# Kernel optimization log

Hardware: AMD Instinct MI355X
Metric: run time of the kernel (lower is better)

Reference implementation:

```python
import jax, jax.numpy as jnp
import numpy as np

BITS = 4
OFF = 8          # 2**(BITS-1)
QLEVELS = 15.0   # 2**BITS - 1
IN_F, OUT_F, FP_F, TOKENS = 4096, 4096, 256, 4096
INT_F = IN_F - FP_F


def unpack_i4(w_packed):
    """Invert pack_to_i4: packed uint8 col k holds signed int4 cols (2k: low nibble, 2k+1: high)."""
    lo = (w_packed & 0x0F).astype(jnp.int8)
    hi = ((w_packed >> 4) & 0x0F).astype(jnp.int8)
    lo = jnp.where(lo >= 8, lo - 16, lo)
    hi = jnp.where(hi >= 8, hi - 16, hi)
    return jnp.stack([lo, hi], axis=-1).reshape(w_packed.shape[0], -1)  # (out, int_features)


def setup_inputs() -> dict:
    key = jax.random.key(0)
    k1, k2, k3, k4, k5 = jax.random.split(key, 5)
    x = jax.random.normal(k1, (1, TOKENS, IN_F), dtype=jnp.float16)
    perm = jax.random.permutation(k2, IN_F)
    fp_indices = jnp.sort(perm[:FP_F]).astype(jnp.int64)
    int_indices = jnp.sort(perm[FP_F:]).astype(jnp.int64)
    # signed int4 weight values in [-8, 7], packed two-per-byte like pack_to_i4
    w_vals = jax.random.randint(k3, (OUT_F, INT_F), -8, 8, dtype=jnp.int8)
    u = (w_vals.astype(jnp.int32) & 0x0F).astype(jnp.uint8)
    int_weight = (u[:, 0::2] | (u[:, 1::2] << 4)).astype(jnp.uint8)  # (out, INT_F//2)
    weights_scales = (jax.random.uniform(k4, (OUT_F, 1)) * 0.01 + 1e-3).astype(jnp.float16)
    # reduced_w = row-sum of the dequantized int-column weights (as in from_float)
    reduced_w = (w_vals.astype(jnp.float32).sum(axis=1, keepdims=True)
                 * weights_scales.astype(jnp.float32)).T.astype(jnp.float16)  # (1, out)
    fp_weight = (jax.random.normal(k5, (OUT_F, FP_F)) * 0.02).astype(jnp.float16)
    bias = jnp.zeros((OUT_F,), dtype=jnp.float16)
    return {"x": x, "int_weight": int_weight, "weights_scales": weights_scales,
            "reduced_w": reduced_w, "fp_weight": fp_weight, "bias": bias,
            "int_indices": int_indices, "fp_indices": fp_indices}


def reference(x, int_weight, weights_scales, reduced_w, fp_weight, bias,
              int_indices, fp_indices):
    x2 = x[0]                                   # (M, in_features)
    int_x = x2[:, int_indices].astype(jnp.float32)   # (M, INT_F)
    fp_x = x2[:, fp_indices].astype(jnp.float32)     # (M, FP_F)
    # asymmetric per-row quantization to signed int4
    mn = int_x.min(axis=1, keepdims=True)
    mx = int_x.max(axis=1, keepdims=True)
    scale = jnp.maximum((mx - mn) / QLEVELS, 1e-8)   # (M,1)
    zero = mn                                        # (M,1)
    q = jnp.clip(jnp.round((int_x - zero) / scale) - OFF, -8, 7).astype(jnp.int8)
    w_int = unpack_i4(int_weight)                    # (out, INT_F) int8
    int_result = jnp.matmul(q.astype(jnp.int32), w_int.T.astype(jnp.int32))  # (M, out) int32
    fp_result = fp_x @ fp_weight.T.astype(jnp.float32) + bias.astype(jnp.float32)
    # asym dequant: x ~ (q + OFF)*scale + zero, W = w_int * w_scale, sum_j W_j = reduced_w
    w_scale = weights_scales.astype(jnp.float32)[:, 0][None, :]   # (1, out)
    out = (scale * w_scale * int_result.astype(jnp.float32)
           + (zero + scale * OFF) * reduced_w.astype(jnp.float32)
           + fp_result)
    return out.astype(jnp.float16)[None]             # (1, M, out)
```

## Files before the change

### kernel.cpp

```cpp
#include <hip/hip_runtime.h>
#include <hip/hip_bf16.h>

#define IN_FEAT 4096
#define OUT_FEAT 4096
#define FP_FEAT 256
#define INT_FEAT 3840
#define TOKENS 4096
#define PACKED_W (INT_FEAT / 2)

#define NT_I8 60
#define NT_ALL 68

typedef __attribute__((ext_vector_type(8))) short short8;
typedef __attribute__((ext_vector_type(4))) float f32x4;
typedef __attribute__((ext_vector_type(4))) int   int32x4;

#define AQ8_OFF   0u
#define WB8_OFF   16777216u
#define AFP_OFF   33554432u
#define WFP_OFF   35651584u
#define SCALE_OFF 37748736u
#define ZERO_OFF  37765120u
#define WS_NEED   37781504u

__global__ __launch_bounds__(256) void prep_kernel(
    const float* __restrict__ x,
    const int* __restrict__ int_idx_raw,
    const int* __restrict__ fp_idx_raw,
    const int* __restrict__ wpacked_raw,
    const float* __restrict__ fpw,
    const float* __restrict__ wscale,
    signed char* __restrict__ Aq8,
    __hip_bfloat16* __restrict__ Afp,
    signed char* __restrict__ Wb8,
    __hip_bfloat16* __restrict__ Wfp,
    float* __restrict__ scale_ws,
    float* __restrict__ zero_ws)
{
    const int t = threadIdx.x;
    if (blockIdx.x < TOKENS) {
        const int m = blockIdx.x;
        const float* xr = x + (size_t)m * IN_FEAT;
        const bool is64 = (int_idx_raw[1] == 0) && (int_idx_raw[3] == 0);

        float v[15];
        float mn = 1e30f, mx = -1e30f;
#pragma unroll
        for (int j = 0; j < 15; ++j) {
            int k = t + j * 256;
            int idx = is64 ? int_idx_raw[2 * k] : int_idx_raw[k];
            float f = xr[idx];
            v[j] = f;
            mn = fminf(mn, f);
            mx = fmaxf(mx, f);
        }
#pragma unroll
        for (int off = 1; off < 64; off <<= 1) {
            mn = fminf(mn, __shfl_xor(mn, off));
            mx = fmaxf(mx, __shfl_xor(mx, off));
        }
        __shared__ float smn[4], smx[4];
        int wid = t >> 6, lane = t & 63;
        if (lane == 0) { smn[wid] = mn; smx[wid] = mx; }
        __syncthreads();
        if (t == 0) {
            float rmn = fminf(fminf(smn[0], smn[1]), fminf(smn[2], smn[3]));
            float rmx = fmaxf(fmaxf(smx[0], smx[1]), fmaxf(smx[2], smx[3]));
            float sc = fmaxf((rmx - rmn) / 15.0f, 1e-8f);
            smn[0] = rmn;
            smx[0] = sc;
            scale_ws[m] = sc;
            zero_ws[m] = rmn;
        }
        __syncthreads();
        const float zero = smn[0];
        const float sc = smx[0];

        signed char* ar = Aq8 + (size_t)m * INT_FEAT;
#pragma unroll
        for (int j = 0; j < 15; ++j) {
            int k = t + j * 256;
            float q = rintf((v[j] - zero) / sc) - 8.0f;
            q = fminf(fmaxf(q, -8.0f), 7.0f);
            ar[k] = (signed char)(int)q;
        }
        int fpi = is64 ? fp_idx_raw[2 * t] : fp_idx_raw[t];
        Afp[(size_t)m * FP_FEAT + t] = __float2bfloat16(xr[fpi] / sc);
    } else {
        const int n = blockIdx.x - TOKENS;
        bool is_i32 = true;
#pragma unroll
        for (int j = 0; j < 8; ++j) {
            unsigned w = (unsigned)wpacked_raw[j];
            if (w > 0xFFu) is_i32 = false;
        }
        short* wo = (short*)(Wb8 + (size_t)n * INT_FEAT);
#pragma unroll
        for (int j = 0; j < 8; ++j) {
            int k = t + j * 256;
            if (k < PACKED_W) {
                int p = is_i32 ? wpacked_raw[(size_t)n * PACKED_W + k]
                               : ((const unsigned char*)wpacked_raw)[(size_t)n * PACKED_W + k];
                int lo = p & 15; if (lo >= 8) lo -= 16;
                int hi = (p >> 4) & 15; if (hi >= 8) hi -= 16;
                wo[k] = (short)(((unsigned char)lo) | ((unsigned short)(unsigned char)hi << 8));
            }
        }
        float wsn = wscale[n];
        Wfp[(size_t)n * FP_FEAT + t] = __float2bfloat16(fpw[(size_t)n * FP_FEAT + t] / wsn);
    }
}


__global__ __launch_bounds__(512, 2) void gemm256_i8(
    const signed char* __restrict__ Aq8,
    const __hip_bfloat16* __restrict__ Afp,
    const signed char* __restrict__ Wb8,
    const __hip_bfloat16* __restrict__ Wfp,
    const float* __restrict__ scale_ws,
    const float* __restrict__ zero_ws,
    const float* __restrict__ wscale,
    const float* __restrict__ reduced,
    const float* __restrict__ bias,
    float* __restrict__ out)
{
    __shared__ __align__(16) char lds[131072];

    const int t = threadIdx.x;
    const int lane = t & 63, wid = t >> 6;
    const int wr = wid >> 2;
    const int wc = wid & 3;
    const int r16 = lane & 15;
    const int kg = lane >> 4;

    const int bid = blockIdx.x;
    const int sb = (bid & 7) * 32 + (bid >> 3);
    const int tileM = (sb >> 4) * 256;
    const int tileN = (sb & 15) * 256;

    const int id0 = t, id1 = 512 + t;
    const int r0 = id0 >> 2, c0 = id0 & 3;
    const int r1 = id1 >> 2, c1 = id1 & 3;
    const int sw0 = ((c0 ^ ((r0 >> 1) & 3)) << 4);
    const int sw1 = ((c1 ^ ((r1 >> 1) & 3)) << 4);
    const char* a8_0 = (const char*)Aq8 + (size_t)(tileM + r0) * INT_FEAT + sw0;
    const char* a8_1 = (const char*)Aq8 + (size_t)(tileM + r1) * INT_FEAT + sw1;
    const char* b8_0 = (const char*)Wb8 + (size_t)(tileN + r0) * INT_FEAT + sw0;
    const char* b8_1 = (const char*)Wb8 + (size_t)(tileN + r1) * INT_FEAT + sw1;
    const char* af_0 = (const char*)Afp + (size_t)(tileM + r0) * 512 + sw0;
    const char* af_1 = (const char*)Afp + (size_t)(tileM + r1) * 512 + sw1;
    const char* bf_0 = (const char*)Wfp + (size_t)(tileN + r0) * 512 + sw0;
    const char* bf_1 = (const char*)Wfp + (size_t)(tileN + r1) * 512 + sw1;
    const int dst0 = id0 << 4, dst1 = id1 << 4;

    auto stage = [&](int vt, int bufB) {
        const char *pa0, *pa1, *pb0, *pb1;
        if (vt < NT_I8) {
            int ko = vt * 64;
            pa0 = a8_0 + ko; pa1 = a8_1 + ko; pb0 = b8_0 + ko; pb1 = b8_1 + ko;
        } else {
            int ko = (vt - NT_I8) * 64;
            pa0 = af_0 + ko; pa1 = af_1 + ko; pb0 = bf_0 + ko; pb1 = bf_1 + ko;
        }
        __builtin_amdgcn_global_load_lds(
            (const __attribute__((address_space(1))) void*)pa0,
            (__attribute__((address_space(3))) void*)(lds + bufB + dst0), 16, 0, 0);
        __builtin_amdgcn_global_load_lds(
            (const __attribute__((address_space(1))) void*)pa1,
            (__attribute__((address_space(3))) void*)(lds + bufB + dst1), 16, 0, 0);
        __builtin_amdgcn_global_load_lds(
            (const __attribute__((address_space(1))) void*)pb0,
            (__attribute__((address_space(3))) void*)(lds + bufB + 16384 + dst0), 16, 0, 0);
        __builtin_amdgcn_global_load_lds(
            (const __attribute__((address_space(1))) void*)pb1,
            (__attribute__((address_space(3))) void*)(lds + bufB + 16384 + dst1), 16, 0, 0);
    };

    int aOff[8], bOff[4];
#pragma unroll
    for (int mf = 0; mf < 8; ++mf) {
        int ra = wr * 128 + mf * 16 + r16;
        aOff[mf] = ra * 64 + ((((ra >> 1) & 3) ^ kg) << 4);
    }
#pragma unroll
    for (int nf = 0; nf < 4; ++nf) {
        int rb = wc * 64 + nf * 16 + r16;
        bOff[nf] = 16384 + rb * 64 + ((((rb >> 1) & 3) ^ kg) << 4);
    }

    int32x4 acc[8][4];
#pragma unroll
    for (int mf = 0; mf < 8; ++mf)
#pragma unroll
        for (int nf = 0; nf < 4; ++nf)
            acc[mf][nf] = (int32x4){0, 0, 0, 0};

    stage(0, 0);
    stage(1, 32768);
    stage(2, 65536);
    asm volatile("s_waitcnt vmcnt(8)" ::: "memory");
    __builtin_amdgcn_sched_barrier(0);
    __builtin_amdgcn_s_barrier();
    __builtin_amdgcn_sched_barrier(0);

    for (int vt = 0; vt < NT_I8; ++vt) {
        const int bufB = (vt & 3) << 15;
        int32x4 bI[4], aI[8];
#pragma unroll
        for (int nf = 0; nf < 4; ++nf)
            bI[nf] = *(const int32x4*)(lds + bufB + bOff[nf]);
#pragma unroll
        for (int mf = 0; mf < 8; ++mf)
            aI[mf] = *(const int32x4*)(lds + bufB + aOff[mf]);

        stage(vt + 3, ((vt + 3) & 3) << 15);

        __builtin_amdgcn_s_setprio(1);
#pragma unroll
        for (int mf = 0; mf < 8; ++mf)
#pragma unroll
            for (int nf = 0; nf < 4; ++nf)
                acc[mf][nf] = __builtin_amdgcn_mfma_i32_16x16x64_i8(
                    aI[mf], bI[nf], acc[mf][nf], 0, 0, 0);
        __builtin_amdgcn_s_setprio(0);

        asm volatile("s_waitcnt vmcnt(8)" ::: "memory");
        __builtin_amdgcn_sched_barrier(0);
        __builtin_amdgcn_s_barrier();
        __builtin_amdgcn_sched_barrier(0);
    }

#pragma unroll
    for (int mf = 0; mf < 8; ++mf)
#pragma unroll
        for (int nf = 0; nf < 4; ++nf) {
            int32x4 vi = acc[mf][nf];
            f32x4 vf;
#pragma unroll
            for (int i = 0; i < 4; ++i) vf[i] = (float)vi[i];
            acc[mf][nf] = __builtin_bit_cast(int32x4, vf);
        }

    for (int vt = NT_I8; vt < NT_ALL; ++vt) {
        const int bufB = (vt & 3) << 15;
        short8 bF[4], aF[8];
#pragma unroll
        for (int nf = 0; nf < 4; ++nf)
            bF[nf] = *(const short8*)(lds + bufB + bOff[nf]);
#pragma unroll
        for (int mf = 0; mf < 8; ++mf)
            aF[mf] = *(const short8*)(lds + bufB + aOff[mf]);

        if (vt + 3 < NT_ALL)
            stage(vt + 3, ((vt + 3) & 3) << 15);

        __builtin_amdgcn_s_setprio(1);
#pragma unroll
        for (int mf = 0; mf < 8; ++mf)
#pragma unroll
            for (int nf = 0; nf < 4; ++nf)
                acc[mf][nf] = __builtin_bit_cast(int32x4,
                    __builtin_amdgcn_mfma_f32_16x16x32_bf16(
                        aF[mf], bF[nf],
                        __builtin_bit_cast(f32x4, acc[mf][nf]), 0, 0, 0));
        __builtin_amdgcn_s_setprio(0);

        if (vt <= NT_ALL - 4)
            asm volatile("s_waitcnt vmcnt(8)" ::: "memory");
        else if (vt == NT_ALL - 3)
            asm volatile("s_waitcnt vmcnt(4)" ::: "memory");
        else if (vt == NT_ALL - 2)
            asm volatile("s_waitcnt vmcnt(0)" ::: "memory");
        __builtin_amdgcn_sched_barrier(0);
        __builtin_amdgcn_s_barrier();
        __builtin_amdgcn_sched_barrier(0);
    }

    const int cr4 = kg * 4;
#pragma unroll
    for (int mf = 0; mf < 8; ++mf) {
#pragma unroll
        for (int nf = 0; nf < 4; ++nf) {
            int n = tileN + wc * 64 + nf * 16 + r16;
            float ws = wscale[n];
            float rd = reduced[n];
            float bs = bias[n];
            f32x4 av = __builtin_bit_cast(f32x4, acc[mf][nf]);
#pragma unroll
            for (int i = 0; i < 4; ++i) {
                int m = tileM + wr * 128 + mf * 16 + cr4 + i;
                float sc = scale_ws[m];
                float zr = zero_ws[m];
                out[(size_t)m * OUT_FEAT + n] =
                    sc * ws * av[i]
                    + (zr + sc * 8.0f) * rd + bs;
            }
        }
    }
}

extern "C" void kernel_launch(void* const* d_in, const int* in_sizes, int n_in,
                              void* d_out, int out_size, void* d_ws, size_t ws_size,
                              hipStream_t stream)
{
    const void* px = 0; const void* pw = 0; const void* pfpw = 0;
    const void* pii = 0; const void* pfi = 0;
    const void* p4096[3] = {0, 0, 0}; int n4096 = 0;
    for (int i = 0; i < n_in; ++i) {
        switch (in_sizes[i]) {
            case 16777216: px = d_in[i]; break;
            case 7864320:  pw = d_in[i]; break;
            case 1048576:  pfpw = d_in[i]; break;
            case 3840:     pii = d_in[i]; break;
            case 256:      pfi = d_in[i]; break;
            case 4096:     if (n4096 < 3) p4096[n4096++] = d_in[i]; break;
            default: break;
        }
    }
    if (!px || !pw || !pfpw || !pii || !pfi || n4096 != 3) return;

    const float* x       = (const float*)px;
    const int*   wpacked = (const int*)pw;
    const float* wscale  = (const float*)p4096[0];
    const float* reduced = (const float*)p4096[1];
    const float* bias    = (const float*)p4096[2];
    const float* fpw     = (const float*)pfpw;
    const int*   int_idx = (const int*)pii;
    const int*   fp_idx  = (const int*)pfi;
    float*       out     = (float*)d_out;

    if (ws_size < (size_t)WS_NEED) return;

    char* ws = (char*)d_ws;
    signed char*    Aq8 = (signed char*)(ws + AQ8_OFF);
    signed char*    Wb8 = (signed char*)(ws + WB8_OFF);
    __hip_bfloat16* Afp = (__hip_bfloat16*)(ws + AFP_OFF);
    __hip_bfloat16* Wfp = (__hip_bfloat16*)(ws + WFP_OFF);
    float* scale_ws     = (float*)(ws + SCALE_OFF);
    float* zero_ws      = (float*)(ws + ZERO_OFF);

    prep_kernel<<<TOKENS + OUT_FEAT, 256, 0, stream>>>(
        x, int_idx, fp_idx, wpacked, fpw, wscale,
        Aq8, Afp, Wb8, Wfp, scale_ws, zero_ws);
    gemm256_i8<<<256, 512, 0, stream>>>(Aq8, Afp, Wb8, Wfp,
                                        scale_ws, zero_ws,
                                        wscale, reduced, bias, out);
}
```

Measured before the change: 98.71 us.

## Split int8 main loop into four interleaved phases with per-phase prefetch and barriers

The int8 K-loop is split into four phases. Each phase reads two A fragments from LDS, issues one of the four global-to-LDS prefetch loads, then runs eight MFMAs, with s_barrier placed around each phase. The goal is to interleave LDS reads, global prefetch and MFMA work across waves in a ping-pong style, and to lower register pressure by holding only two A fragments at a time. The cost is eight barriers per iteration instead of one, which may add synchronisation overhead. It also moves the vmcnt wait into the last phase, before that phase's barrier.

```diff
diff --git a/kernel.cpp b/kernel.cpp
--- a/kernel.cpp
+++ b/kernel.cpp
@@ -153,27 +153,19 @@
     const char* bf_1 = (const char*)Wfp + (size_t)(tileN + r1) * 512 + sw1;
     const int dst0 = id0 << 4, dst1 = id1 << 4;
 
-    auto stage = [&](int vt, int bufB) {
-        const char *pa0, *pa1, *pb0, *pb1;
-        if (vt < NT_I8) {
-            int ko = vt * 64;
-            pa0 = a8_0 + ko; pa1 = a8_1 + ko; pb0 = b8_0 + ko; pb1 = b8_1 + ko;
-        } else {
-            int ko = (vt - NT_I8) * 64;
-            pa0 = af_0 + ko; pa1 = af_1 + ko; pb0 = bf_0 + ko; pb1 = bf_1 + ko;
+    auto stage_one = [&](int vt, int bufB, int j) {
+        const bool i8p = vt < NT_I8;
+        const int ko = i8p ? vt * 64 : (vt - NT_I8) * 64;
+        const char* p; int d;
+        switch (j) {
+            case 0:  p = (i8p ? a8_0 : af_0) + ko; d = dst0;         break;
+            case 1:  p = (i8p ? a8_1 : af_1) + ko; d = dst1;         break;
+            case 2:  p = (i8p ? b8_0 : bf_0) + ko; d = 16384 + dst0; break;
+            default: p = (i8p ? b8_1 : bf_1) + ko; d = 16384 + dst1; break;
         }
         __builtin_amdgcn_global_load_lds(
-            (const __attribute__((address_space(1))) void*)pa0,
-            (__attribute__((address_space(3))) void*)(lds + bufB + dst0), 16, 0, 0);
-        __builtin_amdgcn_global_load_lds(
-            (const __attribute__((address_space(1))) void*)pa1,
-            (__attribute__((address_space(3))) void*)(lds + bufB + dst1), 16, 0, 0);
-        __builtin_amdgcn_global_load_lds(
-            (const __attribute__((address_space(1))) void*)pb0,
-            (__attribute__((address_space(3))) void*)(lds + bufB + 16384 + dst0), 16, 0, 0);
-        __builtin_amdgcn_global_load_lds(
-            (const __attribute__((address_space(1))) void*)pb1,
-            (__attribute__((address_space(3))) void*)(lds + bufB + 16384 + dst1), 16, 0, 0);
+            (const __attribute__((address_space(1))) void*)p,
+            (__attribute__((address_space(3))) void*)(lds + bufB + d), 16, 0, 0);
     };
 
     int aOff[8], bOff[4];
@@ -195,40 +187,69 @@
         for (int nf = 0; nf < 4; ++nf)
             acc[mf][nf] = (int32x4){0, 0, 0, 0};
 
-    stage(0, 0);
-    stage(1, 32768);
-    stage(2, 65536);
+#pragma unroll
+    for (int j = 0; j < 4; ++j) stage_one(0, 0, j);
+#pragma unroll
+    for (int j = 0; j < 4; ++j) stage_one(1, 32768, j);
+#pragma unroll
+    for (int j = 0; j < 4; ++j) stage_one(2, 65536, j);
     asm volatile("s_waitcnt vmcnt(8)" ::: "memory");
     __builtin_amdgcn_sched_barrier(0);
     __builtin_amdgcn_s_barrier();
     __builtin_amdgcn_sched_barrier(0);
 
+#define PHASE_I8(P, READS, EXTRA)                                              \
+    do {                                                                       \
+        READS;                                                                 \
+        stage_one(vt + 3, sB, P);                                              \
+        EXTRA;                                                                 \
+        __builtin_amdgcn_s_barrier();                                          \
+        asm volatile("s_waitcnt lgkmcnt(0)" ::: "memory");                     \
+        __builtin_amdgcn_sched_barrier(0);                                     \
+        __builtin_amdgcn_s_setprio(1);                                         \
+        _Pragma("unroll")                                                      \
+        for (int nf = 0; nf < 4; ++nf) {                                       \
+            acc[2*(P)][nf]   = __builtin_amdgcn_mfma_i32_16x16x64_i8(          \
+                aE, bI[nf], acc[2*(P)][nf], 0, 0, 0);                          \
+            acc[2*(P)+1][nf] = __builtin_amdgcn_mfma_i32_16x16x64_i8(          \
+                aO, bI[nf], acc[2*(P)+1][nf], 0, 0, 0);                        \
+        }                                                                      \
+        __builtin_amdgcn_s_setprio(0);                                         \
+        __builtin_amdgcn_s_barrier();                                          \
+    } while (0)
+
     for (int vt = 0; vt < NT_I8; ++vt) {
         const int bufB = (vt & 3) << 15;
-        int32x4 bI[4], aI[8];
-#pragma unroll
-        for (int nf = 0; nf < 4; ++nf)
-            bI[nf] = *(const int32x4*)(lds + bufB + bOff[nf]);
-#pragma unroll
-        for (int mf = 0; mf < 8; ++mf)
-            aI[mf] = *(const int32x4*)(lds + bufB + aOff[mf]);
-
-        stage(vt + 3, ((vt + 3) & 3) << 15);
-
-        __builtin_amdgcn_s_setprio(1);
-#pragma unroll
-        for (int mf = 0; mf < 8; ++mf)
-#pragma unroll
-            for (int nf = 0; nf < 4; ++nf)
-                acc[mf][nf] = __builtin_amdgcn_mfma_i32_16x16x64_i8(
-                    aI[mf], bI[nf], acc[mf][nf], 0, 0, 0);
-        __builtin_amdgcn_s_setprio(0);
-
-        asm volatile("s_waitcnt vmcnt(8)" ::: "memory");
-        __builtin_amdgcn_sched_barrier(0);
-        __builtin_amdgcn_s_barrier();
-        __builtin_amdgcn_sched_barrier(0);
-    }
+        const int sB = ((vt + 3) & 3) << 15;
+        int32x4 bI[4], aE, aO;
+
+        PHASE_I8(0,
+            {
+                bI[0] = *(const int32x4*)(lds + bufB + bOff[0]);
+                bI[1] = *(const int32x4*)(lds + bufB + bOff[1]);
+                bI[2] = *(const int32x4*)(lds + bufB + bOff[2]);
+                bI[3] = *(const int32x4*)(lds + bufB + bOff[3]);
+                aE = *(const int32x4*)(lds + bufB + aOff[0]);
+                aO = *(const int32x4*)(lds + bufB + aOff[1]);
+            }, {});
+        PHASE_I8(1,
+            {
+                aE = *(const int32x4*)(lds + bufB + aOff[2]);
+                aO = *(const int32x4*)(lds + bufB + aOff[3]);
+            }, {});
+        PHASE_I8(2,
+            {
+                aE = *(const int32x4*)(lds + bufB + aOff[4]);
+                aO = *(const int32x4*)(lds + bufB + aOff[5]);
+            }, {});
+        PHASE_I8(3,
+            {
+                aE = *(const int32x4*)(lds + bufB + aOff[6]);
+                aO = *(const int32x4*)(lds + bufB + aOff[7]);
+            },
+            { asm volatile("s_waitcnt vmcnt(8)" ::: "memory"); });
+    }
+#undef PHASE_I8
 
 #pragma unroll
     for (int mf = 0; mf < 8; ++mf)
@@ -243,6 +264,7 @@
 
     for (int vt = NT_I8; vt < NT_ALL; ++vt) {
         const int bufB = (vt & 3) << 15;
+        const int sB = ((vt + 3) & 3) << 15;
         short8 bF[4], aF[8];
 #pragma unroll
         for (int nf = 0; nf < 4; ++nf)
@@ -251,8 +273,10 @@
         for (int mf = 0; mf < 8; ++mf)
             aF[mf] = *(const short8*)(lds + bufB + aOff[mf]);
 
-        if (vt + 3 < NT_ALL)
-            stage(vt + 3, ((vt + 3) & 3) << 15);
+        if (vt + 3 < NT_ALL) {
+#pragma unroll
+            for (int j = 0; j < 4; ++j) stage_one(vt + 3, sB, j);
+        }
 
         __builtin_amdgcn_s_setprio(1);
 #pragma unroll
```

Result: no change. 98.77 us (+0.1%).

## Shrink GEMM tile to 256x128 with triple-buffered LDS and 512 blocks

Applied to the files above, without the earlier changes.

Changes the GEMM tile from 256x256 to 256x128, with 8 waves arranged 4x2, and launches 512 blocks instead of 256 so all CUs on the device are covered. The LDS pipeline drops from a 4-deep to a 3-deep ring of 24 KB stages (72 KB total), and occupancy is raised via launch_bounds(512,4). Per-wave accumulators fall from 32 to 16 tiles, which cuts register pressure. The cost is lower arithmetic intensity (more global and L2 traffic per FLOP) and less prefetch depth to hide memory latency.

```diff
diff --git a/kernel.cpp b/kernel.cpp
--- a/kernel.cpp
+++ b/kernel.cpp
@@ -112,7 +112,7 @@
 }
 
 
-__global__ __launch_bounds__(512, 2) void gemm256_i8(
+__global__ __launch_bounds__(512, 4) void gemm256_i8(
     const signed char* __restrict__ Aq8,
     const __hip_bfloat16* __restrict__ Afp,
     const signed char* __restrict__ Wb8,
@@ -124,62 +124,53 @@
     const float* __restrict__ bias,
     float* __restrict__ out)
 {
-    __shared__ __align__(16) char lds[131072];
+    __shared__ __align__(16) char lds[73728];
 
     const int t = threadIdx.x;
     const int lane = t & 63, wid = t >> 6;
-    const int wr = wid >> 2;
-    const int wc = wid & 3;
+    const int wr = wid >> 1;
+    const int wc = wid & 1;
     const int r16 = lane & 15;
     const int kg = lane >> 4;
 
     const int bid = blockIdx.x;
-    const int sb = (bid & 7) * 32 + (bid >> 3);
-    const int tileM = (sb >> 4) * 256;
-    const int tileN = (sb & 15) * 256;
-
-    const int id0 = t, id1 = 512 + t;
-    const int r0 = id0 >> 2, c0 = id0 & 3;
-    const int r1 = id1 >> 2, c1 = id1 & 3;
+    const int sb = (bid & 7) * 64 + (bid >> 3);
+    const int tileM = (sb >> 5) * 256;
+    const int tileN = (sb & 31) * 128;
+
+    const int r0 = t >> 2, c0 = t & 3;
     const int sw0 = ((c0 ^ ((r0 >> 1) & 3)) << 4);
-    const int sw1 = ((c1 ^ ((r1 >> 1) & 3)) << 4);
     const char* a8_0 = (const char*)Aq8 + (size_t)(tileM + r0) * INT_FEAT + sw0;
-    const char* a8_1 = (const char*)Aq8 + (size_t)(tileM + r1) * INT_FEAT + sw1;
+    const char* a8_1 = (const char*)Aq8 + (size_t)(tileM + 128 + r0) * INT_FEAT + sw0;
     const char* b8_0 = (const char*)Wb8 + (size_t)(tileN + r0) * INT_FEAT + sw0;
-    const char* b8_1 = (const char*)Wb8 + (size_t)(tileN + r1) * INT_FEAT + sw1;
     const char* af_0 = (const char*)Afp + (size_t)(tileM + r0) * 512 + sw0;
-    const char* af_1 = (const char*)Afp + (size_t)(tileM + r1) * 512 + sw1;
+    const char* af_1 = (const char*)Afp + (size_t)(tileM + 128 + r0) * 512 + sw0;
     const char* bf_0 = (const char*)Wfp + (size_t)(tileN + r0) * 512 + sw0;
-    const char* bf_1 = (const char*)Wfp + (size_t)(tileN + r1) * 512 + sw1;
-    const int dst0 = id0 << 4, dst1 = id1 << 4;
+    const int dstA0 = t << 4;
+    const int dstA1 = (512 + t) << 4;
+    const int dstB0 = t << 4;
 
     auto stage = [&](int vt, int bufB) {
-        const char *pa0, *pa1, *pb0, *pb1;
-        if (vt < NT_I8) {
-            int ko = vt * 64;
-            pa0 = a8_0 + ko; pa1 = a8_1 + ko; pb0 = b8_0 + ko; pb1 = b8_1 + ko;
-        } else {
-            int ko = (vt - NT_I8) * 64;
-            pa0 = af_0 + ko; pa1 = af_1 + ko; pb0 = bf_0 + ko; pb1 = bf_1 + ko;
-        }
+        const bool i8p = vt < NT_I8;
+        const int ko = i8p ? vt * 64 : (vt - NT_I8) * 64;
+        const char* pa0 = (i8p ? a8_0 : af_0) + ko;
+        const char* pa1 = (i8p ? a8_1 : af_1) + ko;
+        const char* pb0 = (i8p ? b8_0 : bf_0) + ko;
         __builtin_amdgcn_global_load_lds(
             (const __attribute__((address_space(1))) void*)pa0,
-            (__attribute__((address_space(3))) void*)(lds + bufB + dst0), 16, 0, 0);
+            (__attribute__((address_space(3))) void*)(lds + bufB + dstA0), 16, 0, 0);
         __builtin_amdgcn_global_load_lds(
             (const __attribute__((address_space(1))) void*)pa1,
-            (__attribute__((address_space(3))) void*)(lds + bufB + dst1), 16, 0, 0);
+            (__attribute__((address_space(3))) void*)(lds + bufB + dstA1), 16, 0, 0);
         __builtin_amdgcn_global_load_lds(
             (const __attribute__((address_space(1))) void*)pb0,
-            (__attribute__((address_space(3))) void*)(lds + bufB + 16384 + dst0), 16, 0, 0);
-        __builtin_amdgcn_global_load_lds(
-            (const __attribute__((address_space(1))) void*)pb1,
-            (__attribute__((address_space(3))) void*)(lds + bufB + 16384 + dst1), 16, 0, 0);
+            (__attribute__((address_space(3))) void*)(lds + bufB + 16384 + dstB0), 16, 0, 0);
     };
 
-    int aOff[8], bOff[4];
-#pragma unroll
-    for (int mf = 0; mf < 8; ++mf) {
-        int ra = wr * 128 + mf * 16 + r16;
+    int aOff[4], bOff[4];
+#pragma unroll
+    for (int mf = 0; mf < 4; ++mf) {
+        int ra = wr * 64 + mf * 16 + r16;
         aOff[mf] = ra * 64 + ((((ra >> 1) & 3) ^ kg) << 4);
     }
 #pragma unroll
@@ -188,50 +179,50 @@
         bOff[nf] = 16384 + rb * 64 + ((((rb >> 1) & 3) ^ kg) << 4);
     }
 
-    int32x4 acc[8][4];
-#pragma unroll
-    for (int mf = 0; mf < 8; ++mf)
+    int32x4 acc[4][4];
+#pragma unroll
+    for (int mf = 0; mf < 4; ++mf)
 #pragma unroll
         for (int nf = 0; nf < 4; ++nf)
             acc[mf][nf] = (int32x4){0, 0, 0, 0};
 
     stage(0, 0);
-    stage(1, 32768);
-    stage(2, 65536);
-    asm volatile("s_waitcnt vmcnt(8)" ::: "memory");
+    stage(1, 24576);
+    asm volatile("s_waitcnt vmcnt(3)" ::: "memory");
     __builtin_amdgcn_sched_barrier(0);
     __builtin_amdgcn_s_barrier();
     __builtin_amdgcn_sched_barrier(0);
 
+    int bufB = 0;
     for (int vt = 0; vt < NT_I8; ++vt) {
-        const int bufB = (vt & 3) << 15;
-        int32x4 bI[4], aI[8];
+        int32x4 bI[4], aI[4];
 #pragma unroll
         for (int nf = 0; nf < 4; ++nf)
             bI[nf] = *(const int32x4*)(lds + bufB + bOff[nf]);
 #pragma unroll
-        for (int mf = 0; mf < 8; ++mf)
+        for (int mf = 0; mf < 4; ++mf)
             aI[mf] = *(const int32x4*)(lds + bufB + aOff[mf]);
 
-        stage(vt + 3, ((vt + 3) & 3) << 15);
+        stage(vt + 2, (bufB == 0) ? 49152 : bufB - 24576);
 
         __builtin_amdgcn_s_setprio(1);
 #pragma unroll
-        for (int mf = 0; mf < 8; ++mf)
+        for (int mf = 0; mf < 4; ++mf)
 #pragma unroll
             for (int nf = 0; nf < 4; ++nf)
                 acc[mf][nf] = __builtin_amdgcn_mfma_i32_16x16x64_i8(
                     aI[mf], bI[nf], acc[mf][nf], 0, 0, 0);
         __builtin_amdgcn_s_setprio(0);
 
-        asm volatile("s_waitcnt vmcnt(8)" ::: "memory");
+        asm volatile("s_waitcnt vmcnt(3)" ::: "memory");
         __builtin_amdgcn_sched_barrier(0);
         __builtin_amdgcn_s_barrier();
         __builtin_amdgcn_sched_barrier(0);
-    }
-
-#pragma unroll
-    for (int mf = 0; mf < 8; ++mf)
+        bufB = (bufB == 49152) ? 0 : bufB + 24576;
+    }
+
+#pragma unroll
+    for (int mf = 0; mf < 4; ++mf)
 #pragma unroll
         for (int nf = 0; nf < 4; ++nf) {
             int32x4 vi = acc[mf][nf];
@@ -242,21 +233,20 @@
         }
 
     for (int vt = NT_I8; vt < NT_ALL; ++vt) {
-        const int bufB = (vt & 3) << 15;
-        short8 bF[4], aF[8];
+        short8 bF[4], aF[4];
 #pragma unroll
         for (int nf = 0; nf < 4; ++nf)
             bF[nf] = *(const short8*)(lds + bufB + bOff[nf]);
 #pragma unroll
-        for (int mf = 0; mf < 8; ++mf)
+        for (int mf = 0; mf < 4; ++mf)
             aF[mf] = *(const short8*)(lds + bufB + aOff[mf]);
 
-        if (vt + 3 < NT_ALL)
-            stage(vt + 3, ((vt + 3) & 3) << 15);
+        if (vt + 2 < NT_ALL)
+            stage(vt + 2, (bufB == 0) ? 49152 : bufB - 24576);
 
         __builtin_amdgcn_s_setprio(1);
 #pragma unroll
-        for (int mf = 0; mf < 8; ++mf)
+        for (int mf = 0; mf < 4; ++mf)
 #pragma unroll
             for (int nf = 0; nf < 4; ++nf)
                 acc[mf][nf] = __builtin_bit_cast(int32x4,
@@ -265,20 +255,19 @@
                         __builtin_bit_cast(f32x4, acc[mf][nf]), 0, 0, 0));
         __builtin_amdgcn_s_setprio(0);
 
-        if (vt <= NT_ALL - 4)
-            asm volatile("s_waitcnt vmcnt(8)" ::: "memory");
-        else if (vt == NT_ALL - 3)
-            asm volatile("s_waitcnt vmcnt(4)" ::: "memory");
+        if (vt <= NT_ALL - 3)
+            asm volatile("s_waitcnt vmcnt(3)" ::: "memory");
         else if (vt == NT_ALL - 2)
             asm volatile("s_waitcnt vmcnt(0)" ::: "memory");
         __builtin_amdgcn_sched_barrier(0);
         __builtin_amdgcn_s_barrier();
         __builtin_amdgcn_sched_barrier(0);
+        bufB = (bufB == 49152) ? 0 : bufB + 24576;
     }
 
     const int cr4 = kg * 4;
 #pragma unroll
-    for (int mf = 0; mf < 8; ++mf) {
+    for (int mf = 0; mf < 4; ++mf) {
 #pragma unroll
         for (int nf = 0; nf < 4; ++nf) {
             int n = tileN + wc * 64 + nf * 16 + r16;
@@ -288,7 +277,7 @@
             f32x4 av = __builtin_bit_cast(f32x4, acc[mf][nf]);
 #pragma unroll
             for (int i = 0; i < 4; ++i) {
-                int m = tileM + wr * 128 + mf * 16 + cr4 + i;
+                int m = tileM + wr * 64 + mf * 16 + cr4 + i;
                 float sc = scale_ws[m];
                 float zr = zero_ws[m];
                 out[(size_t)m * OUT_FEAT + n] =
@@ -342,7 +331,7 @@
     prep_kernel<<<TOKENS + OUT_FEAT, 256, 0, stream>>>(
         x, int_idx, fp_idx, wpacked, fpw, wscale,
         Aq8, Afp, Wb8, Wfp, scale_ws, zero_ws);
-    gemm256_i8<<<256, 512, 0, stream>>>(Aq8, Afp, Wb8, Wfp,
+    gemm256_i8<<<512, 512, 0, stream>>>(Aq8, Afp, Wb8, Wfp,
                                         scale_ws, zero_ws,
                                         wscale, reduced, bias, out);
 }
```

Result: slower. 110.7 us (+12.2%).

## Load B fragments directly to registers and shrink LDS A-only pipeline

Applied to the files above, without the earlier changes.

The weight (B) tile is no longer staged through LDS. Each wave loads its B fragments straight from global memory into double-buffered registers one tile ahead, while only the A tile goes through LDS. LDS drops from 128KB to 64KB and the prefetch depth falls from three tiles to two. This removes the B LDS writes and reads, at the cost of B reloads across the two wave rows and unswizzled 16-byte global loads, with less latency hiding.

```diff
diff --git a/kernel.cpp b/kernel.cpp
--- a/kernel.cpp
+++ b/kernel.cpp
@@ -112,6 +112,58 @@
 }
 
 
+#define TILE_I8(VT, BUSE, BLOAD)                                               \
+    {                                                                          \
+        const int bufB = ((VT) & 3) << 14;                                     \
+        loadB4((VT) + 1, BLOAD);                                               \
+        stageA((VT) + 2, (((VT) + 2) & 3) << 14);                              \
+        int32x4 aI[8];                                                         \
+        _Pragma("unroll")                                                      \
+        for (int mf = 0; mf < 8; ++mf)                                         \
+            aI[mf] = *(const int32x4*)(lds + bufB + aOff[mf]);                 \
+        asm volatile("s_waitcnt vmcnt(6)" ::: "memory");                       \
+        asm volatile("s_waitcnt lgkmcnt(0)" ::: "memory");                     \
+        __builtin_amdgcn_sched_barrier(0);                                     \
+        __builtin_amdgcn_s_setprio(1);                                         \
+        _Pragma("unroll")                                                      \
+        for (int mf = 0; mf < 8; ++mf)                                         \
+            _Pragma("unroll")                                                  \
+            for (int nf = 0; nf < 4; ++nf)                                     \
+                acc[mf][nf] = __builtin_amdgcn_mfma_i32_16x16x64_i8(           \
+                    aI[mf], (BUSE)[nf], acc[mf][nf], 0, 0, 0);                 \
+        __builtin_amdgcn_s_setprio(0);                                         \
+        __builtin_amdgcn_sched_barrier(0);                                     \
+        __builtin_amdgcn_s_barrier();                                          \
+        __builtin_amdgcn_sched_barrier(0);                                     \
+    }
+
+#define TILE_FP(VT, BUSE, BLOAD, MIDSTR)                                       \
+    {                                                                          \
+        const int bufB = ((VT) & 3) << 14;                                     \
+        if ((VT) + 1 < NT_ALL) loadB4((VT) + 1, BLOAD);                        \
+        if ((VT) + 2 < NT_ALL) stageA((VT) + 2, (((VT) + 2) & 3) << 14);       \
+        short8 aF[8];                                                          \
+        _Pragma("unroll")                                                      \
+        for (int mf = 0; mf < 8; ++mf)                                         \
+            aF[mf] = *(const short8*)(lds + bufB + aOff[mf]);                  \
+        asm volatile("s_waitcnt vmcnt(" MIDSTR ")" ::: "memory");              \
+        asm volatile("s_waitcnt lgkmcnt(0)" ::: "memory");                     \
+        __builtin_amdgcn_sched_barrier(0);                                     \
+        __builtin_amdgcn_s_setprio(1);                                         \
+        _Pragma("unroll")                                                      \
+        for (int mf = 0; mf < 8; ++mf)                                         \
+            _Pragma("unroll")                                                  \
+            for (int nf = 0; nf < 4; ++nf)                                     \
+                acc[mf][nf] = __builtin_bit_cast(int32x4,                      \
+                    __builtin_amdgcn_mfma_f32_16x16x32_bf16(                   \
+                        aF[mf], __builtin_bit_cast(short8, (BUSE)[nf]),        \
+                        __builtin_bit_cast(f32x4, acc[mf][nf]), 0, 0, 0));     \
+        __builtin_amdgcn_s_setprio(0);                                         \
+        __builtin_amdgcn_sched_barrier(0);                                     \
+        __builtin_amdgcn_s_barrier();                                          \
+        __builtin_amdgcn_sched_barrier(0);                                     \
+    }
+
 __global__ __launch_bounds__(512, 2) void gemm256_i8(
     const signed char* __restrict__ Aq8,
     const __hip_bfloat16* __restrict__ Afp,
@@ -124,7 +176,7 @@
     const float* __restrict__ bias,
     float* __restrict__ out)
 {
-    __shared__ __align__(16) char lds[131072];
+    __shared__ __align__(16) char lds[65536];
 
     const int t = threadIdx.x;
     const int lane = t & 63, wid = t >> 6;
@@ -138,55 +190,55 @@
     const int tileM = (sb >> 4) * 256;
     const int tileN = (sb & 15) * 256;
 
-    const int id0 = t, id1 = 512 + t;
-    const int r0 = id0 >> 2, c0 = id0 & 3;
-    const int r1 = id1 >> 2, c1 = id1 & 3;
+    const int r0 = t >> 2, c0 = t & 3;
     const int sw0 = ((c0 ^ ((r0 >> 1) & 3)) << 4);
-    const int sw1 = ((c1 ^ ((r1 >> 1) & 3)) << 4);
     const char* a8_0 = (const char*)Aq8 + (size_t)(tileM + r0) * INT_FEAT + sw0;
-    const char* a8_1 = (const char*)Aq8 + (size_t)(tileM + r1) * INT_FEAT + sw1;
-    const char* b8_0 = (const char*)Wb8 + (size_t)(tileN + r0) * INT_FEAT + sw0;
-    const char* b8_1 = (const char*)Wb8 + (size_t)(tileN + r1) * INT_FEAT + sw1;
+    const char* a8_1 = (const char*)Aq8 + (size_t)(tileM + 128 + r0) * INT_FEAT + sw0;
     const char* af_0 = (const char*)Afp + (size_t)(tileM + r0) * 512 + sw0;
-    const char* af_1 = (const char*)Afp + (size_t)(tileM + r1) * 512 + sw1;
-    const char* bf_0 = (const char*)Wfp + (size_t)(tileN + r0) * 512 + sw0;
-    const char* bf_1 = (const char*)Wfp + (size_t)(tileN + r1) * 512 + sw1;
-    const int dst0 = id0 << 4, dst1 = id1 << 4;
-
-    auto stage = [&](int vt, int bufB) {
-        const char *pa0, *pa1, *pb0, *pb1;
-        if (vt < NT_I8) {
-            int ko = vt * 64;
-            pa0 = a8_0 + ko; pa1 = a8_1 + ko; pb0 = b8_0 + ko; pb1 = b8_1 + ko;
-        } else {
-            int ko = (vt - NT_I8) * 64;
-            pa0 = af_0 + ko; pa1 = af_1 + ko; pb0 = bf_0 + ko; pb1 = bf_1 + ko;
-        }
+    const char* af_1 = (const char*)Afp + (size_t)(tileM + 128 + r0) * 512 + sw0;
+    const int dstA0 = t << 4;
+    const int dstA1 = (512 + t) << 4;
+
+    auto stageA = [&](int vt, int bufB) {
+        const bool i8p = vt < NT_I8;
+        const int ko = i8p ? vt * 64 : (vt - NT_I8) * 64;
+        const char* pa0 = (i8p ? a8_0 : af_0) + ko;
+        const char* pa1 = (i8p ? a8_1 : af_1) + ko;
         __builtin_amdgcn_global_load_lds(
             (const __attribute__((address_space(1))) void*)pa0,
-            (__attribute__((address_space(3))) void*)(lds + bufB + dst0), 16, 0, 0);
+            (__attribute__((address_space(3))) void*)(lds + bufB + dstA0), 16, 0, 0);
         __builtin_amdgcn_global_load_lds(
             (const __attribute__((address_space(1))) void*)pa1,
-            (__attribute__((address_space(3))) void*)(lds + bufB + dst1), 16, 0, 0);
-        __builtin_amdgcn_global_load_lds(
-            (const __attribute__((address_space(1))) void*)pb0,
-            (__attribute__((address_space(3))) void*)(lds + bufB + 16384 + dst0), 16, 0, 0);
-        __builtin_amdgcn_global_load_lds(
-            (const __attribute__((address_space(1))) void*)pb1,
-            (__attribute__((address_space(3))) void*)(lds + bufB + 16384 + dst1), 16, 0, 0);
+            (__attribute__((address_space(3))) void*)(lds + bufB + dstA1), 16, 0, 0);
     };
 
-    int aOff[8], bOff[4];
+    const char* bi8 = (const char*)Wb8
+        + (size_t)(tileN + wc * 64 + r16) * INT_FEAT + kg * 16;
+    const char* bfp = (const char*)Wfp
+        + (size_t)(tileN + wc * 64 + r16) * 512 + kg * 16;
+
+    auto loadB4 = [&](int vt, int32x4* d) {
+        if (vt < NT_I8) {
+            const char* p = bi8 + vt * 64;
+            d[0] = *(const int32x4*)(p);
+            d[1] = *(const int32x4*)(p + 16 * INT_FEAT);
+            d[2] = *(const int32x4*)(p + 32 * INT_FEAT);
+            d[3] = *(const int32x4*)(p + 48 * INT_FEAT);
+        } else {
+            const char* p = bfp + (vt - NT_I8) * 64;
+            d[0] = *(const int32x4*)(p);
+            d[1] = *(const int32x4*)(p + 16 * 512);
+            d[2] = *(const int32x4*)(p + 32 * 512);
+            d[3] = *(const int32x4*)(p + 48 * 512);
+        }
+    };
+
+    int aOff[8];
 #pragma unroll
     for (int mf = 0; mf < 8; ++mf) {
         int ra = wr * 128 + mf * 16 + r16;
         aOff[mf] = ra * 64 + ((((ra >> 1) & 3) ^ kg) << 4);
     }
-#pragma unroll
-    for (int nf = 0; nf < 4; ++nf) {
-        int rb = wc * 64 + nf * 16 + r16;
-        bOff[nf] = 16384 + rb * 64 + ((((rb >> 1) & 3) ^ kg) << 4);
-    }
 
     int32x4 acc[8][4];
 #pragma unroll
@@ -195,39 +247,19 @@
         for (int nf = 0; nf < 4; ++nf)
             acc[mf][nf] = (int32x4){0, 0, 0, 0};
 
-    stage(0, 0);
-    stage(1, 32768);
-    stage(2, 65536);
-    asm volatile("s_waitcnt vmcnt(8)" ::: "memory");
+    int32x4 bA[4], bB[4];
+
+    stageA(0, 0);
+    stageA(1, 16384);
+    loadB4(0, bA);
+    asm volatile("s_waitcnt vmcnt(0)" ::: "memory");
     __builtin_amdgcn_sched_barrier(0);
     __builtin_amdgcn_s_barrier();
     __builtin_amdgcn_sched_barrier(0);
 
-    for (int vt = 0; vt < NT_I8; ++vt) {
-        const int bufB = (vt & 3) << 15;
-        int32x4 bI[4], aI[8];
-#pragma unroll
-        for (int nf = 0; nf < 4; ++nf)
-            bI[nf] = *(const int32x4*)(lds + bufB + bOff[nf]);
-#pragma unroll
-        for (int mf = 0; mf < 8; ++mf)
-            aI[mf] = *(const int32x4*)(lds + bufB + aOff[mf]);
-
-        stage(vt + 3, ((vt + 3) & 3) << 15);
-
-        __builtin_amdgcn_s_setprio(1);
-#pragma unroll
-        for (int mf = 0; mf < 8; ++mf)
-#pragma unroll
-            for (int nf = 0; nf < 4; ++nf)
-                acc[mf][nf] = __builtin_amdgcn_mfma_i32_16x16x64_i8(
-                    aI[mf], bI[nf], acc[mf][nf], 0, 0, 0);
-        __builtin_amdgcn_s_setprio(0);
-
-        asm volatile("s_waitcnt vmcnt(8)" ::: "memory");
-        __builtin_amdgcn_sched_barrier(0);
-        __builtin_amdgcn_s_barrier();
-        __builtin_amdgcn_sched_barrier(0);
+    for (int vt = 0; vt < NT_I8; vt += 2) {
+        TILE_I8(vt, bA, bB);
+        TILE_I8(vt + 1, bB, bA);
     }
 
 #pragma unroll
@@ -241,40 +273,14 @@
             acc[mf][nf] = __builtin_bit_cast(int32x4, vf);
         }
 
-    for (int vt = NT_I8; vt < NT_ALL; ++vt) {
-        const int bufB = (vt & 3) << 15;
-        short8 bF[4], aF[8];
-#pragma unroll
-        for (int nf = 0; nf < 4; ++nf)
-            bF[nf] = *(const short8*)(lds + bufB + bOff[nf]);
-#pragma unroll
-        for (int mf = 0; mf < 8; ++mf)
-            aF[mf] = *(const short8*)(lds + bufB + aOff[mf]);
-
-        if (vt + 3 < NT_ALL)
-            stage(vt + 3, ((vt + 3) & 3) << 15);
-
-        __builtin_amdgcn_s_setprio(1);
-#pragma unroll
-        for (int mf = 0; mf < 8; ++mf)
-#pragma unroll
-            for (int nf = 0; nf < 4; ++nf)
-                acc[mf][nf] = __builtin_bit_cast(int32x4,
-                    __builtin_amdgcn_mfma_f32_16x16x32_bf16(
-                        aF[mf], bF[nf],
-                        __builtin_bit_cast(f32x4, acc[mf][nf]), 0, 0, 0));
-        __builtin_amdgcn_s_setprio(0);
-
-        if (vt <= NT_ALL - 4)
-            asm volatile("s_waitcnt vmcnt(8)" ::: "memory");
-        else if (vt == NT_ALL - 3)
-            asm volatile("s_waitcnt vmcnt(4)" ::: "memory");
-        else if (vt == NT_ALL - 2)
-            asm volatile("s_waitcnt vmcnt(0)" ::: "memory");
-        __builtin_amdgcn_sched_barrier(0);
-        __builtin_amdgcn_s_barrier();
-        __builtin_amdgcn_sched_barrier(0);
-    }
+    TILE_FP(60, bA, bB, "6");
+    TILE_FP(61, bB, bA, "6");
+    TILE_FP(62, bA, bB, "6");
+    TILE_FP(63, bB, bA, "6");
+    TILE_FP(64, bA, bB, "6");
+    TILE_FP(65, bB, bA, "6");
+    TILE_FP(66, bA, bB, "4");
+    TILE_FP(67, bB, bA, "0");
 
     const int cr4 = kg * 4;
 #pragma unroll
```

New measurement: 135.0 us. 1.37x slower.
